# Kernel tuning notes

Hardware: AMD Instinct MI355X
Metric: run time of the kernel (lower is better)

Reference implementation:

```python
import jax, jax.numpy as jnp
import numpy as np

N_NODES = 100000
N_EDGES = 3200000
IN_DIM = 512
HIDDEN = 16
N_CLASSES = 7


def setup_inputs() -> dict:
    key = jax.random.key(0)
    k1, k2, k3, k4 = jax.random.split(key, 4)
    x = jax.random.normal(k1, (N_NODES, IN_DIM), dtype=jnp.float32)
    edge_index = jax.random.randint(k2, (2, N_EDGES), 0, N_NODES, dtype=jnp.int32)
    W1 = jax.random.normal(k3, (IN_DIM, HIDDEN), dtype=jnp.float32) / np.sqrt(IN_DIM)
    b1 = jnp.zeros((HIDDEN,), dtype=jnp.float32)
    W2 = jax.random.normal(k4, (HIDDEN, N_CLASSES), dtype=jnp.float32) / np.sqrt(HIDDEN)
    b2 = jnp.zeros((N_CLASSES,), dtype=jnp.float32)
    return {"x": x, "edge_index": edge_index, "W1": W1, "b1": b1, "W2": W2, "b2": b2}


def _gcn_norm(edge_index, num_nodes):
    # Add self loops and compute symmetric normalization D^{-1/2} A D^{-1/2}
    loop = jnp.arange(num_nodes, dtype=edge_index.dtype)
    src = jnp.concatenate([edge_index[0], loop])
    dst = jnp.concatenate([edge_index[1], loop])
    deg = jax.ops.segment_sum(jnp.ones_like(dst, dtype=jnp.float32), dst,
                              num_segments=num_nodes)
    dinv = jnp.where(deg > 0, jax.lax.rsqrt(deg), 0.0)
    norm = dinv[src] * dinv[dst]  # [E + N]
    return src, dst, norm


def _gcn_conv(x, W, b, src, dst, norm, num_nodes):
    h = x @ W                                   # [N, out] dense GEMM first (PyG order)
    msg = h[src] * norm[:, None]                # gather + per-edge scale
    agg = jax.ops.segment_sum(msg, dst, num_segments=num_nodes)  # scatter-add
    return agg + b


def reference(x, edge_index, W1, b1, W2, b2):
    n = x.shape[0]
    src, dst, norm = _gcn_norm(edge_index, n)
    h = _gcn_conv(x, W1, b1, src, dst, norm, n)
    h = jax.nn.relu(h)
    # dropout is identity in eval mode (deterministic reference)
    out = _gcn_conv(h, W2, b2, src, dst, norm, n)
    return jax.nn.log_softmax(out, axis=1)
```

## Files before the change

### kernel.cpp

```cpp
#include <hip/hip_runtime.h>

#define N_NODES 100000
#define N_EDGES 3200000
#define IN_DIM  512
#define HIDDEN  16
#define NCLS    7

#define BSH     9
#define BNODES  512
#define NB      ((N_NODES + BNODES - 1) / BNODES)

#define EPB1    8192
#define NBLK1   ((N_EDGES + EPB1 - 1) / EPB1)
#define EPB2    4096
#define NBLK2   ((N_EDGES + EPB2 - 1) / EPB2)

#define GEMM1_BLOCKS 512

__global__ void k_zero(int* __restrict__ bcnt, int* __restrict__ rowstart) {
    int i = threadIdx.x;
    bcnt[i] = 0;
    if (i == 0) rowstart[N_NODES] = N_EDGES;
}

__global__ __launch_bounds__(256) void k_bcount(const int* __restrict__ dst,
                                                int* __restrict__ bcnt) {
    __shared__ int hist[256];
    int tid = threadIdx.x;
    hist[tid] = 0;
    __syncthreads();
    int e0 = blockIdx.x * EPB1;
    int n  = min(EPB1, N_EDGES - e0);
    for (int k = tid; k < n; k += 256)
        atomicAdd(&hist[dst[e0 + k] >> BSH], 1);
    __syncthreads();
    int c = hist[tid];
    if (c) atomicAdd(&bcnt[tid], c);
}

__global__ __launch_bounds__(256) void k_bscan(const int* __restrict__ bcnt,
                                               int* __restrict__ bstart,
                                               int* __restrict__ bcur) {
    __shared__ int s[256];
    int tid = threadIdx.x;
    int c = bcnt[tid];
    s[tid] = c;
    __syncthreads();
    for (int off = 1; off < 256; off <<= 1) {
        int t = (tid >= off) ? s[tid - off] : 0;
        __syncthreads();
        s[tid] += t;
        __syncthreads();
    }
    if (tid == 0) bstart[0] = 0;
    bstart[tid + 1] = s[tid];
    bcur[tid]       = s[tid] - c;
}

__global__ __launch_bounds__(256) void k_bscatter(const int* __restrict__ src,
                                                  const int* __restrict__ dst,
                                                  int* __restrict__ bcur,
                                                  unsigned int* __restrict__ ebuf) {
    __shared__ unsigned int pk[EPB2];
    __shared__ unsigned char bb[EPB2];
    __shared__ int hist[256], base[256], lcur[256];
    int tid = threadIdx.x;
    hist[tid] = 0; lcur[tid] = 0;
    __syncthreads();
    int e0 = blockIdx.x * EPB2;
    int n  = min(EPB2, N_EDGES - e0);
    for (int k = tid; k < n; k += 256) {
        int d = dst[e0 + k];
        int b = d >> BSH;
        pk[k] = ((unsigned int)src[e0 + k] << BSH) | (unsigned int)(d & (BNODES - 1));
        bb[k] = (unsigned char)b;
        atomicAdd(&hist[b], 1);
    }
    __syncthreads();
    int h = hist[tid];
    base[tid] = h ? atomicAdd(&bcur[tid], h) : 0;
    __syncthreads();
    for (int k = tid; k < n; k += 256) {
        int b = bb[k];
        int pos = atomicAdd(&lcur[b], 1);
        ebuf[base[b] + pos] = pk[k];
    }
}

__global__ __launch_bounds__(512) void k_bsort(const int* __restrict__ bstart,
                                               const unsigned int* __restrict__ ebuf,
                                               int* __restrict__ rowstart,
                                               float* __restrict__ dinv,
                                               int* __restrict__ csr_src) {
    __shared__ int hist[512], cur[512];
    int tid = threadIdx.x;
    int b   = blockIdx.x;
    int e0 = bstart[b], e1 = bstart[b + 1];
    hist[tid] = 0;
    __syncthreads();
    for (int i = e0 + tid; i < e1; i += 512)
        atomicAdd(&hist[ebuf[i] & (BNODES - 1)], 1);
    __syncthreads();
    int deg = hist[tid];
    for (int off = 1; off < 512; off <<= 1) {
        int t = (tid >= off) ? hist[tid - off] : 0;
        __syncthreads();
        hist[tid] += t;
        __syncthreads();
    }
    int excl = hist[tid] - deg;
    int node = (b << BSH) + tid;
    if (node < N_NODES) {
        rowstart[node] = e0 + excl;
        dinv[node]     = rsqrtf((float)(deg + 1));
    }
    cur[tid] = excl;
    __syncthreads();
    for (int i = e0 + tid; i < e1; i += 512) {
        unsigned int p = ebuf[i];
        int pos = atomicAdd(&cur[p & (BNODES - 1)], 1);
        csr_src[e0 + pos] = (int)(p >> BSH);
    }
}

__global__ __launch_bounds__(256, 2) void k_gemm1(
    const float* __restrict__ x, const float* __restrict__ W1,
    const float* __restrict__ dinv, float* __restrict__ h1s) {
    const int tid = threadIdx.x;
    const int l   = tid & 63;
    const int wid = blockIdx.x * 4 + (tid >> 6);
    const int nw  = GEMM1_BLOCKS * 4;

    float w[8][16];
#pragma unroll
    for (int q = 0; q < 4; ++q) {
#pragma unroll
        for (int c = 0; c < 4; ++c) {
            float4 t0 = *(const float4*)(W1 + (size_t)(4 * l + q) * 16 + 4 * c);
            w[q][4*c+0] = t0.x; w[q][4*c+1] = t0.y; w[q][4*c+2] = t0.z; w[q][4*c+3] = t0.w;
            float4 t1 = *(const float4*)(W1 + (size_t)(256 + 4 * l + q) * 16 + 4 * c);
            w[4+q][4*c+0] = t1.x; w[4+q][4*c+1] = t1.y; w[4+q][4*c+2] = t1.z; w[4+q][4*c+3] = t1.w;
        }
    }

    const int b0 = l & 1, b1 = (l >> 1) & 1, b2 = (l >> 2) & 1, b3 = (l >> 3) & 1;

    int n = wid;
    if (n >= N_NODES) return;
    const float* xr = x + (size_t)n * IN_DIM;
    float4 v0 = *(const float4*)(xr + 4 * l);
    float4 v1 = *(const float4*)(xr + 256 + 4 * l);

    for (;;) {
        int n2 = n + nw;
        int np = (n2 < N_NODES) ? n2 : n;
        const float* xp = x + (size_t)np * IN_DIM;
        float4 u0 = *(const float4*)(xp + 4 * l);
        float4 u1 = *(const float4*)(xp + 256 + 4 * l);

        float p[16];
#pragma unroll
        for (int j = 0; j < 16; ++j) {
            float a = v0.x * w[0][j];
            a = fmaf(v0.y, w[1][j], a);
            a = fmaf(v0.z, w[2][j], a);
            a = fmaf(v0.w, w[3][j], a);
            a = fmaf(v1.x, w[4][j], a);
            a = fmaf(v1.y, w[5][j], a);
            a = fmaf(v1.z, w[6][j], a);
            a = fmaf(v1.w, w[7][j], a);
            p[j] = a;
        }

        float q8[8];
#pragma unroll
        for (int m = 0; m < 8; ++m) {
            float keep = b0 ? p[2*m+1] : p[2*m];
            float give = b0 ? p[2*m]   : p[2*m+1];
            q8[m] = keep + __shfl_xor(give, 1);
        }
        float r4[4];
#pragma unroll
        for (int t = 0; t < 4; ++t) {
            float keep = b1 ? q8[2*t+1] : q8[2*t];
            float give = b1 ? q8[2*t]   : q8[2*t+1];
            r4[t] = keep + __shfl_xor(give, 2);
        }
        float s2[2];
#pragma unroll
        for (int u = 0; u < 2; ++u) {
            float keep = b2 ? r4[2*u+1] : r4[2*u];
            float give = b2 ? r4[2*u]   : r4[2*u+1];
            s2[u] = keep + __shfl_xor(give, 4);
        }
        float t0 = (b3 ? s2[1] : s2[0]) + __shfl_xor(b3 ? s2[0] : s2[1], 8);
        t0 += __shfl_xor(t0, 16);
        t0 += __shfl_xor(t0, 32);

        float di = dinv[n];
        if (l < 16) h1s[(size_t)n * 16 + l] = t0 * di;

        n = n2;
        if (n >= N_NODES) break;
        v0 = u0; v1 = u1;
    }
}

__global__ __launch_bounds__(256) void k_agg1(
    const int* __restrict__ rowstart, const int* __restrict__ csr_src,
    const float* __restrict__ h1s, const float* __restrict__ dinv,
    const float* __restrict__ b1, float* __restrict__ z) {
    int gid = blockIdx.x * 256 + threadIdx.x;
    int g = gid >> 4, j = gid & 15;
    bool valid = g < N_NODES;
    int n = valid ? g : (N_NODES - 1);
    int start = rowstart[n], end = rowstart[n + 1];
    float acc = h1s[(size_t)n * 16 + j];
#pragma unroll 4
    for (int i = start; i < end; ++i) {
        int s = csr_src[i];
        acc += h1s[(size_t)s * 16 + j];
    }
    if (valid) {
        float v = dinv[n] * acc + b1[j];
        z[(size_t)n * 16 + j] = fmaxf(v, 0.f);
    }
}

__global__ __launch_bounds__(256) void k_layer2(
    const float* __restrict__ z, const float* __restrict__ W2,
    const float* __restrict__ dinv, float* __restrict__ h2s) {
    int n = blockIdx.x * 256 + threadIdx.x;
    if (n >= N_NODES) return;
    float zv[16];
#pragma unroll
    for (int k = 0; k < 16; k += 4) {
        float4 v = *(const float4*)(z + (size_t)n * 16 + k);
        zv[k] = v.x; zv[k+1] = v.y; zv[k+2] = v.z; zv[k+3] = v.w;
    }
    float di = dinv[n];
    float o[8];
#pragma unroll
    for (int jj = 0; jj < 7; ++jj) {
        float a = 0.f;
#pragma unroll
        for (int k = 0; k < 16; ++k) a = fmaf(zv[k], W2[k * 7 + jj], a);
        o[jj] = a * di;
    }
    o[7] = 0.f;
    *(float4*)(h2s + (size_t)n * 8 + 0) = make_float4(o[0], o[1], o[2], o[3]);
    *(float4*)(h2s + (size_t)n * 8 + 4) = make_float4(o[4], o[5], o[6], o[7]);
}

__global__ __launch_bounds__(256) void k_agg2(
    const int* __restrict__ rowstart, const int* __restrict__ csr_src,
    const float* __restrict__ h2s, const float* __restrict__ dinv,
    const float* __restrict__ b2, float* __restrict__ out) {
    int gid = blockIdx.x * 256 + threadIdx.x;
    int g = gid >> 3, j = gid & 7;
    bool valid = g < N_NODES;
    int n = valid ? g : (N_NODES - 1);
    int start = rowstart[n], end = rowstart[n + 1];
    float acc = h2s[(size_t)n * 8 + j];
#pragma unroll 4
    for (int i = start; i < end; ++i) {
        int s = csr_src[i];
        acc += h2s[(size_t)s * 8 + j];
    }
    float v = dinv[n] * acc + ((j < 7) ? b2[j] : -1e30f);
    float m = v;
    m = fmaxf(m, __shfl_xor(m, 1));
    m = fmaxf(m, __shfl_xor(m, 2));
    m = fmaxf(m, __shfl_xor(m, 4));
    float e = (j < 7) ? expf(v - m) : 0.f;
    float ssum = e;
    ssum += __shfl_xor(ssum, 1);
    ssum += __shfl_xor(ssum, 2);
    ssum += __shfl_xor(ssum, 4);
    float ls = logf(ssum) + m;
    if (valid && j < 7) out[(size_t)n * 7 + j] = v - ls;
}

extern "C" void kernel_launch(void* const* d_in, const int* in_sizes, int n_in,
                              void* d_out, int out_size, void* d_ws, size_t ws_size,
                              hipStream_t stream) {
    const float* x  = (const float*)d_in[0];
    const int*   ei = (const int*)d_in[1];
    const float* W1 = (const float*)d_in[2];
    const float* b1 = (const float*)d_in[3];
    const float* W2 = (const float*)d_in[4];
    const float* b2 = (const float*)d_in[5];
    float* out = (float*)d_out;

    const int* src = ei;
    const int* dst = ei + N_EDGES;

    char* ws = (char*)d_ws;
    size_t o = 0;
    auto alloc = [&](size_t bytes) -> void* {
        void* p = ws + o;
        o = (o + bytes + 255) & ~(size_t)255;
        return p;
    };
    int*   bcnt     = (int*)alloc(256 * 4);
    int*   bstart   = (int*)alloc(257 * 4);
    int*   bcur     = (int*)alloc(256 * 4);
    int*   rowstart = (int*)alloc(((size_t)N_NODES + 1) * 4);
    float* dinv     = (float*)alloc((size_t)N_NODES * 4);
    int*   csr_src  = (int*)alloc((size_t)N_EDGES * 4);
    char*  uni      = (char*)alloc((size_t)N_EDGES * 4);
    unsigned int* ebuf = (unsigned int*)uni;
    float* h1s      = (float*)uni;
    float* z        = h1s + (size_t)N_NODES * 16;
    float* h2s      = (float*)alloc((size_t)N_NODES * 8 * 4);

    const int nb_n = (N_NODES + 255) / 256;

    k_zero    <<<1, 256, 0, stream>>>(bcnt, rowstart);
    k_bcount  <<<NBLK1, 256, 0, stream>>>(dst, bcnt);
    k_bscan   <<<1, 256, 0, stream>>>(bcnt, bstart, bcur);
    k_bscatter<<<NBLK2, 256, 0, stream>>>(src, dst, bcur, ebuf);
    k_bsort   <<<NB, 512, 0, stream>>>(bstart, ebuf, rowstart, dinv, csr_src);
    k_gemm1   <<<GEMM1_BLOCKS, 256, 0, stream>>>(x, W1, dinv, h1s);
    k_agg1    <<<(N_NODES * 16 + 255) / 256, 256, 0, stream>>>(rowstart, csr_src, h1s, dinv, b1, z);
    k_layer2  <<<nb_n, 256, 0, stream>>>(z, W2, dinv, h2s);
    k_agg2    <<<(N_NODES * 8 + 255) / 256, 256, 0, stream>>>(rowstart, csr_src, h2s, dinv, b2, out);
}
```

Measured before the change: 462.7 us.

## Replace full CSR sort with bucketed shared-memory atomic aggregation

Drops the per-node CSR sort, so edges stay in 128-node buckets and each block aggregates its bucket into LDS with shared atomics. Layer-1 aggregation, ReLU and the layer-2 matmul are fused into one kernel, and layer-2 aggregation plus log-softmax use the same bucketed scheme. This removes the csr_src write and reread, the rowstart pass and an intermediate z buffer. The cost is LDS atomic contention and a change in float summation order, with the bucket count growing to about 782.

```diff
diff --git a/kernel.cpp b/kernel.cpp
--- a/kernel.cpp
+++ b/kernel.cpp
@@ -6,8 +6,8 @@
 #define HIDDEN  16
 #define NCLS    7
 
-#define BSH     9
-#define BNODES  512
+#define BSH     7
+#define BNODES  128
 #define NB      ((N_NODES + BNODES - 1) / BNODES)
 
 #define EPB1    8192
@@ -17,44 +17,55 @@
 
 #define GEMM1_BLOCKS 512
 
-__global__ void k_zero(int* __restrict__ bcnt, int* __restrict__ rowstart) {
-    int i = threadIdx.x;
-    bcnt[i] = 0;
-    if (i == 0) rowstart[N_NODES] = N_EDGES;
+__global__ void k_zero(int* __restrict__ bcnt) {
+    bcnt[threadIdx.x] = 0;
 }
 
 __global__ __launch_bounds__(256) void k_bcount(const int* __restrict__ dst,
                                                 int* __restrict__ bcnt) {
-    __shared__ int hist[256];
-    int tid = threadIdx.x;
-    hist[tid] = 0;
+    __shared__ int hist[1024];
+    int tid = threadIdx.x;
+#pragma unroll
+    for (int q = 0; q < 4; ++q) hist[q * 256 + tid] = 0;
     __syncthreads();
     int e0 = blockIdx.x * EPB1;
     int n  = min(EPB1, N_EDGES - e0);
     for (int k = tid; k < n; k += 256)
         atomicAdd(&hist[dst[e0 + k] >> BSH], 1);
     __syncthreads();
-    int c = hist[tid];
-    if (c) atomicAdd(&bcnt[tid], c);
+    for (int b = tid; b < NB; b += 256) {
+        int c = hist[b];
+        if (c) atomicAdd(&bcnt[b], c);
+    }
 }
 
 __global__ __launch_bounds__(256) void k_bscan(const int* __restrict__ bcnt,
                                                int* __restrict__ bstart,
                                                int* __restrict__ bcur) {
-    __shared__ int s[256];
-    int tid = threadIdx.x;
-    int c = bcnt[tid];
-    s[tid] = c;
+    __shared__ int ssum[256];
+    int tid = threadIdx.x;
+    int a[4];
+#pragma unroll
+    for (int k = 0; k < 4; ++k) {
+        int idx = tid * 4 + k;
+        a[k] = (idx < NB) ? bcnt[idx] : 0;
+    }
+    int s = a[0] + a[1] + a[2] + a[3];
+    ssum[tid] = s;
     __syncthreads();
     for (int off = 1; off < 256; off <<= 1) {
-        int t = (tid >= off) ? s[tid - off] : 0;
+        int t = (tid >= off) ? ssum[tid - off] : 0;
         __syncthreads();
-        s[tid] += t;
+        ssum[tid] += t;
         __syncthreads();
     }
-    if (tid == 0) bstart[0] = 0;
-    bstart[tid + 1] = s[tid];
-    bcur[tid]       = s[tid] - c;
+    int run = ssum[tid] - s;
+#pragma unroll
+    for (int k = 0; k < 4; ++k) {
+        int idx = tid * 4 + k;
+        if (idx < NB) { bstart[idx] = run; bcur[idx] = run; run += a[k]; }
+    }
+    if (tid == 0) bstart[NB] = N_EDGES;
 }
 
 __global__ __launch_bounds__(256) void k_bscatter(const int* __restrict__ src,
@@ -62,10 +73,11 @@
                                                   int* __restrict__ bcur,
                                                   unsigned int* __restrict__ ebuf) {
     __shared__ unsigned int pk[EPB2];
-    __shared__ unsigned char bb[EPB2];
-    __shared__ int hist[256], base[256], lcur[256];
-    int tid = threadIdx.x;
-    hist[tid] = 0; lcur[tid] = 0;
+    __shared__ unsigned short bb[EPB2];
+    __shared__ int hist[1024], base[1024], lcur[1024];
+    int tid = threadIdx.x;
+#pragma unroll
+    for (int q = 0; q < 4; ++q) { hist[q * 256 + tid] = 0; lcur[q * 256 + tid] = 0; }
     __syncthreads();
     int e0 = blockIdx.x * EPB2;
     int n  = min(EPB2, N_EDGES - e0);
@@ -73,12 +85,14 @@
         int d = dst[e0 + k];
         int b = d >> BSH;
         pk[k] = ((unsigned int)src[e0 + k] << BSH) | (unsigned int)(d & (BNODES - 1));
-        bb[k] = (unsigned char)b;
+        bb[k] = (unsigned short)b;
         atomicAdd(&hist[b], 1);
     }
     __syncthreads();
-    int h = hist[tid];
-    base[tid] = h ? atomicAdd(&bcur[tid], h) : 0;
+    for (int b = tid; b < NB; b += 256) {
+        int h = hist[b];
+        base[b] = h ? atomicAdd(&bcur[b], h) : 0;
+    }
     __syncthreads();
     for (int k = tid; k < n; k += 256) {
         int b = bb[k];
@@ -87,39 +101,21 @@
     }
 }
 
-__global__ __launch_bounds__(512) void k_bsort(const int* __restrict__ bstart,
-                                               const unsigned int* __restrict__ ebuf,
-                                               int* __restrict__ rowstart,
-                                               float* __restrict__ dinv,
-                                               int* __restrict__ csr_src) {
-    __shared__ int hist[512], cur[512];
+__global__ __launch_bounds__(256) void k_deginv(const int* __restrict__ bstart,
+                                                const unsigned int* __restrict__ ebuf,
+                                                float* __restrict__ dinv) {
+    __shared__ int hist[BNODES];
     int tid = threadIdx.x;
     int b   = blockIdx.x;
+    if (tid < BNODES) hist[tid] = 0;
+    __syncthreads();
     int e0 = bstart[b], e1 = bstart[b + 1];
-    hist[tid] = 0;
-    __syncthreads();
-    for (int i = e0 + tid; i < e1; i += 512)
+    for (int i = e0 + tid; i < e1; i += 256)
         atomicAdd(&hist[ebuf[i] & (BNODES - 1)], 1);
     __syncthreads();
-    int deg = hist[tid];
-    for (int off = 1; off < 512; off <<= 1) {
-        int t = (tid >= off) ? hist[tid - off] : 0;
-        __syncthreads();
-        hist[tid] += t;
-        __syncthreads();
-    }
-    int excl = hist[tid] - deg;
-    int node = (b << BSH) + tid;
-    if (node < N_NODES) {
-        rowstart[node] = e0 + excl;
-        dinv[node]     = rsqrtf((float)(deg + 1));
-    }
-    cur[tid] = excl;
-    __syncthreads();
-    for (int i = e0 + tid; i < e1; i += 512) {
-        unsigned int p = ebuf[i];
-        int pos = atomicAdd(&cur[p & (BNODES - 1)], 1);
-        csr_src[e0 + pos] = (int)(p >> BSH);
+    if (tid < BNODES) {
+        int node = b * BNODES + tid;
+        if (node < N_NODES) dinv[node] = rsqrtf((float)(hist[tid] + 1));
     }
 }
 
@@ -206,79 +202,94 @@
     }
 }
 
-__global__ __launch_bounds__(256) void k_agg1(
-    const int* __restrict__ rowstart, const int* __restrict__ csr_src,
+__global__ __launch_bounds__(256) void k_bagg1(
+    const int* __restrict__ bstart, const unsigned int* __restrict__ ebuf,
     const float* __restrict__ h1s, const float* __restrict__ dinv,
-    const float* __restrict__ b1, float* __restrict__ z) {
-    int gid = blockIdx.x * 256 + threadIdx.x;
-    int g = gid >> 4, j = gid & 15;
-    bool valid = g < N_NODES;
-    int n = valid ? g : (N_NODES - 1);
-    int start = rowstart[n], end = rowstart[n + 1];
-    float acc = h1s[(size_t)n * 16 + j];
-#pragma unroll 4
-    for (int i = start; i < end; ++i) {
-        int s = csr_src[i];
-        acc += h1s[(size_t)s * 16 + j];
-    }
-    if (valid) {
-        float v = dinv[n] * acc + b1[j];
-        z[(size_t)n * 16 + j] = fmaxf(v, 0.f);
-    }
-}
-
-__global__ __launch_bounds__(256) void k_layer2(
-    const float* __restrict__ z, const float* __restrict__ W2,
-    const float* __restrict__ dinv, float* __restrict__ h2s) {
-    int n = blockIdx.x * 256 + threadIdx.x;
-    if (n >= N_NODES) return;
-    float zv[16];
-#pragma unroll
-    for (int k = 0; k < 16; k += 4) {
-        float4 v = *(const float4*)(z + (size_t)n * 16 + k);
-        zv[k] = v.x; zv[k+1] = v.y; zv[k+2] = v.z; zv[k+3] = v.w;
-    }
-    float di = dinv[n];
-    float o[8];
-#pragma unroll
-    for (int jj = 0; jj < 7; ++jj) {
-        float a = 0.f;
-#pragma unroll
-        for (int k = 0; k < 16; ++k) a = fmaf(zv[k], W2[k * 7 + jj], a);
-        o[jj] = a * di;
-    }
-    o[7] = 0.f;
-    *(float4*)(h2s + (size_t)n * 8 + 0) = make_float4(o[0], o[1], o[2], o[3]);
-    *(float4*)(h2s + (size_t)n * 8 + 4) = make_float4(o[4], o[5], o[6], o[7]);
-}
-
-__global__ __launch_bounds__(256) void k_agg2(
-    const int* __restrict__ rowstart, const int* __restrict__ csr_src,
+    const float* __restrict__ b1, const float* __restrict__ W2,
+    float* __restrict__ h2s) {
+    __shared__ float acc[BNODES * 16];
+    __shared__ float w2s[16 * 8];
+    int tid = threadIdx.x;
+    int b   = blockIdx.x;
+#pragma unroll
+    for (int q = 0; q < 8; ++q) acc[q * 256 + tid] = 0.f;
+    if (tid < 128) {
+        int k = tid >> 3, jj = tid & 7;
+        w2s[tid] = (jj < 7) ? W2[k * 7 + jj] : 0.f;
+    }
+    __syncthreads();
+
+    int e0 = bstart[b], e1 = bstart[b + 1];
+    int g = tid >> 4, lane = tid & 15;
+    for (int i = e0 + g; i < e1; i += 16) {
+        unsigned int p = ebuf[i];
+        int s   = (int)(p >> BSH);
+        int dlo = (int)(p & (BNODES - 1));
+        float v = h1s[(size_t)s * 16 + lane];
+        atomicAdd(&acc[dlo * 16 + lane], v);
+    }
+    __syncthreads();
+
+    for (int idx = tid; idx < BNODES * 16; idx += 256) {
+        int dlo = idx >> 4, j = idx & 15;
+        int node = b * BNODES + dlo;
+        if (node < N_NODES) {
+            float t = acc[idx] + h1s[(size_t)node * 16 + j];
+            acc[idx] = fmaxf(dinv[node] * t + b1[j], 0.f);
+        }
+    }
+    __syncthreads();
+
+    for (int idx = tid; idx < BNODES * 8; idx += 256) {
+        int dlo = idx >> 3, jj = idx & 7;
+        int node = b * BNODES + dlo;
+        if (node < N_NODES) {
+            float a = 0.f;
+#pragma unroll
+            for (int k = 0; k < 16; ++k) a = fmaf(acc[dlo * 16 + k], w2s[k * 8 + jj], a);
+            h2s[(size_t)node * 8 + jj] = (jj < 7) ? a * dinv[node] : 0.f;
+        }
+    }
+}
+
+__global__ __launch_bounds__(256) void k_bagg2(
+    const int* __restrict__ bstart, const unsigned int* __restrict__ ebuf,
     const float* __restrict__ h2s, const float* __restrict__ dinv,
     const float* __restrict__ b2, float* __restrict__ out) {
-    int gid = blockIdx.x * 256 + threadIdx.x;
-    int g = gid >> 3, j = gid & 7;
-    bool valid = g < N_NODES;
-    int n = valid ? g : (N_NODES - 1);
-    int start = rowstart[n], end = rowstart[n + 1];
-    float acc = h2s[(size_t)n * 8 + j];
-#pragma unroll 4
-    for (int i = start; i < end; ++i) {
-        int s = csr_src[i];
-        acc += h2s[(size_t)s * 8 + j];
-    }
-    float v = dinv[n] * acc + ((j < 7) ? b2[j] : -1e30f);
-    float m = v;
-    m = fmaxf(m, __shfl_xor(m, 1));
-    m = fmaxf(m, __shfl_xor(m, 2));
-    m = fmaxf(m, __shfl_xor(m, 4));
-    float e = (j < 7) ? expf(v - m) : 0.f;
-    float ssum = e;
-    ssum += __shfl_xor(ssum, 1);
-    ssum += __shfl_xor(ssum, 2);
-    ssum += __shfl_xor(ssum, 4);
-    float ls = logf(ssum) + m;
-    if (valid && j < 7) out[(size_t)n * 7 + j] = v - ls;
+    __shared__ float acc[BNODES * 8];
+    int tid = threadIdx.x;
+    int b   = blockIdx.x;
+#pragma unroll
+    for (int q = 0; q < 4; ++q) acc[q * 256 + tid] = 0.f;
+    __syncthreads();
+
+    int e0 = bstart[b], e1 = bstart[b + 1];
+    int g = tid >> 3, lane = tid & 7;
+    for (int i = e0 + g; i < e1; i += 32) {
+        unsigned int p = ebuf[i];
+        int s   = (int)(p >> BSH);
+        int dlo = (int)(p & (BNODES - 1));
+        atomicAdd(&acc[dlo * 8 + lane], h2s[(size_t)s * 8 + lane]);
+    }
+    __syncthreads();
+
+    for (int dlo = g; dlo < BNODES; dlo += 32) {
+        int node = b * BNODES + dlo;
+        if (node >= N_NODES) continue;
+        float tot = acc[dlo * 8 + lane] + h2s[(size_t)node * 8 + lane];
+        float v = dinv[node] * tot + ((lane < 7) ? b2[lane] : -1e30f);
+        float m = v;
+        m = fmaxf(m, __shfl_xor(m, 1));
+        m = fmaxf(m, __shfl_xor(m, 2));
+        m = fmaxf(m, __shfl_xor(m, 4));
+        float e = (lane < 7) ? expf(v - m) : 0.f;
+        float ssum = e;
+        ssum += __shfl_xor(ssum, 1);
+        ssum += __shfl_xor(ssum, 2);
+        ssum += __shfl_xor(ssum, 4);
+        float ls = logf(ssum) + m;
+        if (lane < 7) out[(size_t)node * 7 + lane] = v - ls;
+    }
 }
 
 extern "C" void kernel_launch(void* const* d_in, const int* in_sizes, int n_in,
@@ -302,27 +313,20 @@
         o = (o + bytes + 255) & ~(size_t)255;
         return p;
     };
-    int*   bcnt     = (int*)alloc(256 * 4);
-    int*   bstart   = (int*)alloc(257 * 4);
-    int*   bcur     = (int*)alloc(256 * 4);
-    int*   rowstart = (int*)alloc(((size_t)N_NODES + 1) * 4);
+    int*   bcnt     = (int*)alloc(1024 * 4);
+    int*   bstart   = (int*)alloc(1025 * 4);
+    int*   bcur     = (int*)alloc(1024 * 4);
     float* dinv     = (float*)alloc((size_t)N_NODES * 4);
-    int*   csr_src  = (int*)alloc((size_t)N_EDGES * 4);
-    char*  uni      = (char*)alloc((size_t)N_EDGES * 4);
-    unsigned int* ebuf = (unsigned int*)uni;
-    float* h1s      = (float*)uni;
-    float* z        = h1s + (size_t)N_NODES * 16;
+    unsigned int* ebuf = (unsigned int*)alloc((size_t)N_EDGES * 4);
+    float* h1s      = (float*)alloc((size_t)N_NODES * 16 * 4);
     float* h2s      = (float*)alloc((size_t)N_NODES * 8 * 4);
 
-    const int nb_n = (N_NODES + 255) / 256;
-
-    k_zero    <<<1, 256, 0, stream>>>(bcnt, rowstart);
+    k_zero    <<<1, 1024, 0, stream>>>(bcnt);
     k_bcount  <<<NBLK1, 256, 0, stream>>>(dst, bcnt);
     k_bscan   <<<1, 256, 0, stream>>>(bcnt, bstart, bcur);
     k_bscatter<<<NBLK2, 256, 0, stream>>>(src, dst, bcur, ebuf);
-    k_bsort   <<<NB, 512, 0, stream>>>(bstart, ebuf, rowstart, dinv, csr_src);
+    k_deginv  <<<NB, 256, 0, stream>>>(bstart, ebuf, dinv);
     k_gemm1   <<<GEMM1_BLOCKS, 256, 0, stream>>>(x, W1, dinv, h1s);
-    k_agg1    <<<(N_NODES * 16 + 255) / 256, 256, 0, stream>>>(rowstart, csr_src, h1s, dinv, b1, z);
-    k_layer2  <<<nb_n, 256, 0, stream>>>(z, W2, dinv, h2s);
-    k_agg2    <<<(N_NODES * 8 + 255) / 256, 256, 0, stream>>>(rowstart, csr_src, h2s, dinv, b2, out);
-}
+    k_bagg1   <<<NB, 256, 0, stream>>>(bstart, ebuf, h1s, dinv, b1, W2, h2s);
+    k_bagg2   <<<NB, 256, 0, stream>>>(bstart, ebuf, h2s, dinv, b2, out);
+}
```

Result: slower. 892.9 us (+93.0%).
